# Performance work log

Hardware: AMD Instinct MI355X
Metric: run time of the kernel (lower is better)

Reference implementation:

```python
import jax, jax.numpy as jnp
import numpy as np

B, T, C, H, E, TOP_K = 4, 2048, 1024, 4096, 8, 2


def setup_inputs() -> dict:
    key = jax.random.key(0)
    k0, k1, k2, k3 = jax.random.split(key, 4)
    x = jax.random.normal(k0, (B, T, C), dtype=jnp.float32)
    Wr = jax.random.normal(k1, (C, E), dtype=jnp.float32) * (C ** -0.5)   # router
    W1 = jax.random.normal(k2, (E, C, H), dtype=jnp.float32) * (C ** -0.5)  # expert up-proj
    W2 = jax.random.normal(k3, (E, H, C), dtype=jnp.float32) * (H ** -0.5)  # expert down-proj
    return {"x": x, "Wr": Wr, "W1": W1, "W2": W2}


def reference(x, Wr, W1, W2):
    # x: (B, T, C) -> flatten to tokens, as the wrapper does (n_tokens = B*T)
    Bx, Tx, Cx = x.shape
    flat = x.reshape(-1, Cx)                      # (N, C)
    N = flat.shape[0]

    # --- routing (forward_topk): top-k gates, normalized (is_shared=False) ---
    logits = flat @ Wr                            # (N, E)
    top_vals, top_idx = jax.lax.top_k(logits, TOP_K)   # (N, k)
    gates = jax.nn.softmax(top_vals, axis=-1)     # normalizer = softmax over selected

    # dense combine matrix: gate weight per (token, expert), zero if not routed
    comb = jnp.zeros((N, E), dtype=flat.dtype)
    comb = comb.at[jnp.arange(N)[:, None], top_idx].set(gates)  # (N, E)

    # --- expert FFNs + weighted scatter-add combine ---
    def body(acc, params):
        W1e, W2e, we = params                     # (C,H), (H,C), (N,)
        h = jax.nn.gelu(flat @ W1e)               # (N, H)
        return acc + we[:, None] * (h @ W2e), None

    out, _ = jax.lax.scan(body, jnp.zeros_like(flat), (W1, W2, comb.T))
    return out.reshape(Bx, Tx, Cx)
```

## Files before the change

kernel.cpp:

```cpp
#include <hip/hip_runtime.h>

#define N_TOK 8192
#define CDIM  1024
#define HDIM  4096
#define NEXP  8
#define TOPK  2
#define ROWS  (N_TOK*TOPK)

#define BM 128
#define BN 128
#define BK 64
#define LDK 72

typedef short short8 __attribute__((ext_vector_type(8)));
typedef float floatx4 __attribute__((ext_vector_type(4)));

__device__ __forceinline__ unsigned short f2bf(float f){
  union { float f; unsigned int u; } v; v.f = f;
  unsigned int u = v.u;
  return (unsigned short)((u + 0x7fffu + ((u >> 16) & 1u)) >> 16);
}

__device__ __forceinline__ float gelu_tanh(float x){
  float u = 0.7978845608028654f * (x + 0.044715f * x * x * x);
  float s = __fdividef(1.f, 1.f + __expf(-2.f * u));
  return x * s;
}

__global__ void transpose_cast(const float* __restrict__ src,
                               unsigned short* __restrict__ dst,
                               int roff, int RP, int lds_, int coff, int CP,
                               size_t srcEsz){
  __shared__ __align__(16) unsigned short tile[64][72];
  const int e = blockIdx.z;
  const float* s = src + (size_t)e * srcEsz;
  unsigned short* d = dst + (size_t)e * (size_t)RP * (size_t)CP;
  const int c0 = blockIdx.x * 64, r0 = blockIdx.y * 64;
  const int tid = threadIdx.x;
  #pragma unroll
  for (int i = 0; i < 2; i++){
    int r  = (tid >> 3) + i * 32;
    int cc = (tid & 7) * 8;
    const float* p = s + (size_t)(roff + r0 + r) * lds_ + coff + c0 + cc;
    float4 v0 = *(const float4*)p;
    float4 v1 = *(const float4*)(p + 4);
    unsigned short t8[8];
    t8[0]=f2bf(v0.x); t8[1]=f2bf(v0.y); t8[2]=f2bf(v0.z); t8[3]=f2bf(v0.w);
    t8[4]=f2bf(v1.x); t8[5]=f2bf(v1.y); t8[6]=f2bf(v1.z); t8[7]=f2bf(v1.w);
    *(uint4*)&tile[r][cc] = *(uint4*)t8;
  }
  __syncthreads();
  #pragma unroll
  for (int i = 0; i < 2; i++){
    int oc = (tid >> 3) + i * 32;
    int rr = (tid & 7) * 8;
    unsigned short tmp[8];
    #pragma unroll
    for (int j = 0; j < 8; j++) tmp[j] = tile[rr + j][oc];
    *(uint4*)(d + (size_t)(c0 + oc) * RP + r0 + rr) = *(uint4*)tmp;
  }
}

__global__ void router_topk(const float* __restrict__ x,
                            const float* __restrict__ Wr,
                            int* __restrict__ cnt,
                            int* __restrict__ top_e,
                            float* __restrict__ top_g){
  const int lane = threadIdx.x & 63;
  const int wv   = threadIdx.x >> 6;
  const int t    = blockIdx.x * 4 + wv;
  const float* xr = x + (size_t)t * CDIM;
  float p[NEXP];
  #pragma unroll
  for (int e = 0; e < NEXP; e++) p[e] = 0.f;
  for (int c = lane; c < CDIM; c += 64){
    float xv = xr[c];
    float4 w0 = *(const float4*)(Wr + c * NEXP);
    float4 w1 = *(const float4*)(Wr + c * NEXP + 4);
    p[0] = fmaf(xv, w0.x, p[0]); p[1] = fmaf(xv, w0.y, p[1]);
    p[2] = fmaf(xv, w0.z, p[2]); p[3] = fmaf(xv, w0.w, p[3]);
    p[4] = fmaf(xv, w1.x, p[4]); p[5] = fmaf(xv, w1.y, p[5]);
    p[6] = fmaf(xv, w1.z, p[6]); p[7] = fmaf(xv, w1.w, p[7]);
  }
  #pragma unroll
  for (int e = 0; e < NEXP; e++){
    #pragma unroll
    for (int off = 32; off > 0; off >>= 1)
      p[e] += __shfl_xor(p[e], off, 64);
  }
  if (lane == 0){
    int e0 = 0; float v0 = p[0];
    #pragma unroll
    for (int e = 1; e < NEXP; e++) if (p[e] > v0){ v0 = p[e]; e0 = e; }
    int e1 = -1; float v1 = -1e30f;
    #pragma unroll
    for (int e = 0; e < NEXP; e++) if (e != e0 && p[e] > v1){ v1 = p[e]; e1 = e; }
    float ex  = __expf(v1 - v0);
    float inv = 1.f / (1.f + ex);
    top_e[t * 2 + 0] = e0; top_e[t * 2 + 1] = e1;
    top_g[t * 2 + 0] = inv; top_g[t * 2 + 1] = ex * inv;
    atomicAdd(&cnt[e0], 1);
    atomicAdd(&cnt[e1], 1);
  }
}

__global__ void scan_offsets(const int* __restrict__ cnt,
                             int* __restrict__ off,
                             int* __restrict__ cursor){
  if (threadIdx.x == 0){
    int s = 0;
    for (int e = 0; e < NEXP; e++){ off[e] = s; s += cnt[e]; cursor[e] = 0; }
  }
}

__global__ void assign_rows(const int* __restrict__ off, int* __restrict__ cursor,
                            const int* __restrict__ top_e, const float* __restrict__ top_g,
                            int* __restrict__ tok_of_row, float* __restrict__ gate_of_row){
  int t = blockIdx.x * blockDim.x + threadIdx.x;
  if (t >= N_TOK) return;
  #pragma unroll
  for (int k = 0; k < TOPK; k++){
    int e = top_e[t * 2 + k];
    int pos = atomicAdd(&cursor[e], 1);
    int r = off[e] + pos;
    tok_of_row[r]  = t;
    gate_of_row[r] = top_g[t * 2 + k];
  }
}

__global__ __launch_bounds__(256, 2)
void gemm1_expert(const float* __restrict__ x,
                  const unsigned short* __restrict__ w1t,
                  const int* __restrict__ cnt, const int* __restrict__ off,
                  const int* __restrict__ tok_of_row,
                  unsigned short* __restrict__ hbuf,
                  int HP){
  const int e  = blockIdx.z;
  const int m  = cnt[e];
  const int mt = blockIdx.y;
  if (mt * BM >= m) return;
  const int nt   = blockIdx.x;
  const int base = off[e];

  __shared__ __align__(16) unsigned short As[BM * LDK];
  __shared__ __align__(16) unsigned short Bs[BN * LDK];

  const int tid = threadIdx.x;
  const int lane = tid & 63, wv = tid >> 6;
  const int wm = wv & 1, wn = wv >> 1;
  const int q = lane >> 4, l16 = lane & 15;

  floatx4 acc[4][4];
  #pragma unroll
  for (int i = 0; i < 4; i++)
    #pragma unroll
    for (int j = 0; j < 4; j++) acc[i][j] = (floatx4){0.f, 0.f, 0.f, 0.f};

  const unsigned short* bsrc = w1t + ((size_t)e * HP + (size_t)nt * BN) * CDIM;

  int tokr[4];
  #pragma unroll
  for (int i = 0; i < 4; i++){
    int row  = (tid + i * 256) >> 3;
    int grow = mt * BM + row;
    tokr[i] = tok_of_row[base + (grow < m ? grow : 0)];
  }

  for (int kb = 0; kb < CDIM; kb += BK){
    #pragma unroll
    for (int i = 0; i < 4; i++){
      int chunk = tid + i * 256;
      int row = chunk >> 3;
      int kc  = (chunk & 7) * 8;
      const float* p = x + (size_t)tokr[i] * CDIM + kb + kc;
      float4 v0 = *(const float4*)p;
      float4 v1 = *(const float4*)(p + 4);
      unsigned short t8[8];
      t8[0]=f2bf(v0.x); t8[1]=f2bf(v0.y); t8[2]=f2bf(v0.z); t8[3]=f2bf(v0.w);
      t8[4]=f2bf(v1.x); t8[5]=f2bf(v1.y); t8[6]=f2bf(v1.z); t8[7]=f2bf(v1.w);
      *(uint4*)&As[row * LDK + kc] = *(uint4*)t8;
    }
    #pragma unroll
    for (int i = 0; i < 4; i++){
      int chunk = tid + i * 256;
      int row = chunk >> 3;
      int kc  = (chunk & 7) * 8;
      uint4 v = *(const uint4*)(bsrc + (size_t)row * CDIM + kb + kc);
      *(uint4*)&Bs[row * LDK + kc] = v;
    }
    __syncthreads();
    #pragma unroll
    for (int ks = 0; ks < BK; ks += 32){
      short8 a[4], b[4];
      #pragma unroll
      for (int i = 0; i < 4; i++)
        a[i] = *(const short8*)&As[(wm * 64 + i * 16 + l16) * LDK + ks + q * 8];
      #pragma unroll
      for (int j = 0; j < 4; j++)
        b[j] = *(const short8*)&Bs[(wn * 64 + j * 16 + l16) * LDK + ks + q * 8];
      #pragma unroll
      for (int i = 0; i < 4; i++)
        #pragma unroll
        for (int j = 0; j < 4; j++)
          acc[i][j] = __builtin_amdgcn_mfma_f32_16x16x32_bf16(a[i], b[j], acc[i][j], 0, 0, 0);
    }
    __syncthreads();
  }

  #pragma unroll
  for (int i = 0; i < 4; i++){
    #pragma unroll
    for (int r = 0; r < 4; r++){
      int row  = wm * 64 + i * 16 + q * 4 + r;
      int grow = mt * BM + row;
      if (grow < m){
        size_t hrow = (size_t)(base + grow) * HP + (size_t)nt * BN;
        #pragma unroll
        for (int j = 0; j < 4; j++){
          float g = gelu_tanh(acc[i][j][r]);
          hbuf[hrow + wn * 64 + j * 16 + l16] = f2bf(g);
        }
      }
    }
  }
}

__global__ __launch_bounds__(256, 2)
void gemm2_expert(const unsigned short* __restrict__ hbuf,
                  const unsigned short* __restrict__ w2t,
                  const int* __restrict__ cnt, const int* __restrict__ off,
                  const int* __restrict__ tok_of_row, const float* __restrict__ gate_of_row,
                  float* __restrict__ out,
                  int HP){
  const int e  = blockIdx.z;
  const int m  = cnt[e];
  const int mt = blockIdx.y;
  if (mt * BM >= m) return;
  const int nt   = blockIdx.x;
  const int base = off[e];

  __shared__ __align__(16) unsigned short As[BM * LDK];
  __shared__ __align__(16) unsigned short Bs[BN * LDK];

  const int tid = threadIdx.x;
  const int lane = tid & 63, wv = tid >> 6;
  const int wm = wv & 1, wn = wv >> 1;
  const int q = lane >> 4, l16 = lane & 15;

  floatx4 acc[4][4];
  #pragma unroll
  for (int i = 0; i < 4; i++)
    #pragma unroll
    for (int j = 0; j < 4; j++) acc[i][j] = (floatx4){0.f, 0.f, 0.f, 0.f};

  const unsigned short* bsrc = w2t + ((size_t)e * CDIM + (size_t)nt * BN) * HP;

  int arow[4];
  #pragma unroll
  for (int i = 0; i < 4; i++){
    int row  = (tid + i * 256) >> 3;
    int grow = mt * BM + row;
    arow[i] = base + (grow < m ? grow : 0);
  }

  for (int kb = 0; kb < HP; kb += BK){
    #pragma unroll
    for (int i = 0; i < 4; i++){
      int chunk = tid + i * 256;
      int row = chunk >> 3;
      int kc  = (chunk & 7) * 8;
      uint4 v = *(const uint4*)(hbuf + (size_t)arow[i] * HP + kb + kc);
      *(uint4*)&As[row * LDK + kc] = v;
    }
    #pragma unroll
    for (int i = 0; i < 4; i++){
      int chunk = tid + i * 256;
      int row = chunk >> 3;
      int kc  = (chunk & 7) * 8;
      uint4 v = *(const uint4*)(bsrc + (size_t)row * HP + kb + kc);
      *(uint4*)&Bs[row * LDK + kc] = v;
    }
    __syncthreads();
    #pragma unroll
    for (int ks = 0; ks < BK; ks += 32){
      short8 a[4], b[4];
      #pragma unroll
      for (int i = 0; i < 4; i++)
        a[i] = *(const short8*)&As[(wm * 64 + i * 16 + l16) * LDK + ks + q * 8];
      #pragma unroll
      for (int j = 0; j < 4; j++)
        b[j] = *(const short8*)&Bs[(wn * 64 + j * 16 + l16) * LDK + ks + q * 8];
      #pragma unroll
      for (int i = 0; i < 4; i++)
        #pragma unroll
        for (int j = 0; j < 4; j++)
          acc[i][j] = __builtin_amdgcn_mfma_f32_16x16x32_bf16(a[i], b[j], acc[i][j], 0, 0, 0);
    }
    __syncthreads();
  }

  #pragma unroll
  for (int i = 0; i < 4; i++){
    #pragma unroll
    for (int r = 0; r < 4; r++){
      int row  = wm * 64 + i * 16 + q * 4 + r;
      int grow = mt * BM + row;
      if (grow < m){
        int gr = base + grow;
        int tok = tok_of_row[gr];
        float gate = gate_of_row[gr];
        float* orow = out + (size_t)tok * CDIM + (size_t)nt * BN;
        #pragma unroll
        for (int j = 0; j < 4; j++)
          atomicAdd(&orow[wn * 64 + j * 16 + l16], acc[i][j][r] * gate);
      }
    }
  }
}

extern "C" void kernel_launch(void* const* d_in, const int* in_sizes, int n_in,
                              void* d_out, int out_size, void* d_ws, size_t ws_size,
                              hipStream_t stream) {
  const float* x  = (const float*)d_in[0];
  const float* Wr = (const float*)d_in[1];
  const float* W1 = (const float*)d_in[2];
  const float* W2 = (const float*)d_in[3];
  float* out = (float*)d_out;

  hipMemsetAsync(out, 0, (size_t)N_TOK * CDIM * sizeof(float), stream);

  const size_t META_SZ = 1u << 20;
  int P = -1;
  for (int cand = 1; cand <= 32; cand <<= 1){
    int HPc = HDIM / cand;
    size_t need = META_SZ
                + (size_t)ROWS * HPc * 2
                + (size_t)NEXP * HPc * CDIM * 2;
    if (need <= ws_size){ P = cand; break; }
  }
  if (P < 0){
    return;
  }
  const int HP = HDIM / P;

  char* ws = (char*)d_ws;
  int*   cnt         = (int*)ws;
  int*   off         = cnt + 8;
  int*   cursor      = off + 8;
  int*   tok_of_row  = (int*)(ws + 1024);
  float* gate_of_row = (float*)(ws + 1024 + 65536);
  int*   top_e       = (int*)(ws + 1024 + 131072);
  float* top_g       = (float*)(ws + 1024 + 196608);

  unsigned short* hbuf = (unsigned short*)(ws + META_SZ);
  unsigned short* wreg = (unsigned short*)(ws + META_SZ + (size_t)ROWS * HP * 2);

  hipMemsetAsync(cnt, 0, 96, stream);

  router_topk<<<dim3(N_TOK/4), 256, 0, stream>>>(x, Wr, cnt, top_e, top_g);
  scan_offsets<<<1, 64, 0, stream>>>(cnt, off, cursor);
  assign_rows<<<dim3(N_TOK/256), 256, 0, stream>>>(off, cursor, top_e, top_g,
                                                   tok_of_row, gate_of_row);

  for (int p = 0; p < P; p++){
    const int h0 = p * HP;
    transpose_cast<<<dim3(HP/64, CDIM/64, NEXP), 256, 0, stream>>>(
        W1, wreg, 0, CDIM, HDIM, h0, HP,
        (size_t)CDIM * HDIM);
    gemm1_expert<<<dim3(HP/BN, ROWS/BM, NEXP), 256, 0, stream>>>(
        x, wreg, cnt, off, tok_of_row, hbuf, HP);
    transpose_cast<<<dim3(CDIM/64, HP/64, NEXP), 256, 0, stream>>>(
        W2, wreg, h0, HP, CDIM, 0, CDIM,
        (size_t)HDIM * CDIM);
    gemm2_expert<<<dim3(CDIM/BN, ROWS/BM, NEXP), 256, 0, stream>>>(
        hbuf, wreg, cnt, off, tok_of_row, gate_of_row, out, HP);
  }
}
```

Measured before the change: 1.205 ms.

## Pre-cast x to bf16 and stage GEMM tiles via direct global-to-LDS loads with XOR swizzle

Adds a cast_x kernel that converts x to bf16 once, so gemm1 stops loading fp32 and converting the same token rows in every N-tile block. Both expert GEMMs now fill shared memory with global_load_lds 16-byte direct loads instead of going through registers. The padded LDS layout is replaced by an unpadded one with an XOR swizzle to avoid bank conflicts. This costs an extra workspace buffer and one more kernel launch, and relies on the swizzle matching the MFMA read pattern.

Result: faster. 1.008 ms (-16.3%).

```diff
diff --git a/kernel.cpp b/kernel.cpp
--- a/kernel.cpp
+++ b/kernel.cpp
@@ -10,10 +10,16 @@
 #define BM 128
 #define BN 128
 #define BK 64
-#define LDK 72
 
 typedef short short8 __attribute__((ext_vector_type(8)));
 typedef float floatx4 __attribute__((ext_vector_type(4)));
+
+typedef __attribute__((address_space(3))) unsigned int       as3_u32;
+typedef __attribute__((address_space(1))) const unsigned int as1_u32;
+
+__device__ __forceinline__ void gld16(const unsigned short* g, unsigned short* l){
+  __builtin_amdgcn_global_load_lds((as1_u32*)g, (as3_u32*)l, 16, 0, 0);
+}
 
 __device__ __forceinline__ unsigned short f2bf(float f){
   union { float f; unsigned int u; } v; v.f = f;
@@ -25,6 +31,14 @@
   float u = 0.7978845608028654f * (x + 0.044715f * x * x * x);
   float s = __fdividef(1.f, 1.f + __expf(-2.f * u));
   return x * s;
+}
+
+__global__ void cast_x(const float4* __restrict__ in, uint2* __restrict__ out){
+  int i = blockIdx.x * 256 + threadIdx.x;
+  float4 v = in[i];
+  unsigned short t[4];
+  t[0] = f2bf(v.x); t[1] = f2bf(v.y); t[2] = f2bf(v.z); t[3] = f2bf(v.w);
+  out[i] = *(uint2*)t;
 }
 
 __global__ void transpose_cast(const float* __restrict__ src,
@@ -129,7 +143,7 @@
 }
 
 __global__ __launch_bounds__(256, 2)
-void gemm1_expert(const float* __restrict__ x,
+void gemm1_expert(const unsigned short* __restrict__ xbf,
                   const unsigned short* __restrict__ w1t,
                   const int* __restrict__ cnt, const int* __restrict__ off,
                   const int* __restrict__ tok_of_row,
@@ -142,13 +156,33 @@
   const int nt   = blockIdx.x;
   const int base = off[e];
 
-  __shared__ __align__(16) unsigned short As[BM * LDK];
-  __shared__ __align__(16) unsigned short Bs[BN * LDK];
+  __shared__ __align__(16) unsigned short As[BM * BK];
+  __shared__ __align__(16) unsigned short Bs[BN * BK];
 
   const int tid = threadIdx.x;
-  const int lane = tid & 63, wv = tid >> 6;
-  const int wm = wv & 1, wn = wv >> 1;
+  const int lane = tid & 63, w = tid >> 6;
+  const int wm = w & 1, wn = w >> 1;
   const int q = lane >> 4, l16 = lane & 15;
+  const int sw = l16 & 7;
+
+  const unsigned short* bsrc = w1t + ((size_t)e * HP + (size_t)nt * BN) * CDIM;
+
+  const unsigned short* agp[4];
+  const unsigned short* bgp[4];
+  unsigned short* lA[4];
+  unsigned short* lB[4];
+  #pragma unroll
+  for (int it = 0; it < 4; it++){
+    int r = w * 32 + it * 8 + (lane >> 3);
+    int g = (lane & 7) ^ (r & 7);
+    int grow = mt * BM + r;
+    int cr   = grow < m ? grow : (m - 1);
+    int tok  = tok_of_row[base + cr];
+    agp[it] = xbf + (size_t)tok * CDIM + g * 8;
+    bgp[it] = bsrc + (size_t)r * CDIM + g * 8;
+    lA[it]  = &As[(w * 32 + it * 8) * BK];
+    lB[it]  = &Bs[(w * 32 + it * 8) * BK];
+  }
 
   floatx4 acc[4][4];
   #pragma unroll
@@ -156,48 +190,22 @@
     #pragma unroll
     for (int j = 0; j < 4; j++) acc[i][j] = (floatx4){0.f, 0.f, 0.f, 0.f};
 
-  const unsigned short* bsrc = w1t + ((size_t)e * HP + (size_t)nt * BN) * CDIM;
-
-  int tokr[4];
-  #pragma unroll
-  for (int i = 0; i < 4; i++){
-    int row  = (tid + i * 256) >> 3;
-    int grow = mt * BM + row;
-    tokr[i] = tok_of_row[base + (grow < m ? grow : 0)];
-  }
-
   for (int kb = 0; kb < CDIM; kb += BK){
     #pragma unroll
-    for (int i = 0; i < 4; i++){
-      int chunk = tid + i * 256;
-      int row = chunk >> 3;
-      int kc  = (chunk & 7) * 8;
-      const float* p = x + (size_t)tokr[i] * CDIM + kb + kc;
-      float4 v0 = *(const float4*)p;
-      float4 v1 = *(const float4*)(p + 4);
-      unsigned short t8[8];
-      t8[0]=f2bf(v0.x); t8[1]=f2bf(v0.y); t8[2]=f2bf(v0.z); t8[3]=f2bf(v0.w);
-      t8[4]=f2bf(v1.x); t8[5]=f2bf(v1.y); t8[6]=f2bf(v1.z); t8[7]=f2bf(v1.w);
-      *(uint4*)&As[row * LDK + kc] = *(uint4*)t8;
-    }
-    #pragma unroll
-    for (int i = 0; i < 4; i++){
-      int chunk = tid + i * 256;
-      int row = chunk >> 3;
-      int kc  = (chunk & 7) * 8;
-      uint4 v = *(const uint4*)(bsrc + (size_t)row * CDIM + kb + kc);
-      *(uint4*)&Bs[row * LDK + kc] = v;
-    }
+    for (int it = 0; it < 4; it++) gld16(agp[it] + kb, lA[it]);
+    #pragma unroll
+    for (int it = 0; it < 4; it++) gld16(bgp[it] + kb, lB[it]);
     __syncthreads();
     #pragma unroll
     for (int ks = 0; ks < BK; ks += 32){
+      const int cb = ks >> 3;
       short8 a[4], b[4];
       #pragma unroll
       for (int i = 0; i < 4; i++)
-        a[i] = *(const short8*)&As[(wm * 64 + i * 16 + l16) * LDK + ks + q * 8];
+        a[i] = *(const short8*)&As[(wm * 64 + i * 16 + l16) * BK + (((q + cb) ^ sw) * 8)];
       #pragma unroll
       for (int j = 0; j < 4; j++)
-        b[j] = *(const short8*)&Bs[(wn * 64 + j * 16 + l16) * LDK + ks + q * 8];
+        b[j] = *(const short8*)&Bs[(wn * 64 + j * 16 + l16) * BK + (((q + cb) ^ sw) * 8)];
       #pragma unroll
       for (int i = 0; i < 4; i++)
         #pragma unroll
@@ -217,8 +225,8 @@
         size_t hrow = (size_t)(base + grow) * HP + (size_t)nt * BN;
         #pragma unroll
         for (int j = 0; j < 4; j++){
-          float g = gelu_tanh(acc[i][j][r]);
-          hbuf[hrow + wn * 64 + j * 16 + l16] = f2bf(g);
+          float gv = gelu_tanh(acc[i][j][r]);
+          hbuf[hrow + wn * 64 + j * 16 + l16] = f2bf(gv);
         }
       }
     }
@@ -239,13 +247,32 @@
   const int nt   = blockIdx.x;
   const int base = off[e];
 
-  __shared__ __align__(16) unsigned short As[BM * LDK];
-  __shared__ __align__(16) unsigned short Bs[BN * LDK];
+  __shared__ __align__(16) unsigned short As[BM * BK];
+  __shared__ __align__(16) unsigned short Bs[BN * BK];
 
   const int tid = threadIdx.x;
-  const int lane = tid & 63, wv = tid >> 6;
-  const int wm = wv & 1, wn = wv >> 1;
+  const int lane = tid & 63, w = tid >> 6;
+  const int wm = w & 1, wn = w >> 1;
   const int q = lane >> 4, l16 = lane & 15;
+  const int sw = l16 & 7;
+
+  const unsigned short* bsrc = w2t + ((size_t)e * CDIM + (size_t)nt * BN) * HP;
+
+  const unsigned short* agp[4];
+  const unsigned short* bgp[4];
+  unsigned short* lA[4];
+  unsigned short* lB[4];
+  #pragma unroll
+  for (int it = 0; it < 4; it++){
+    int r = w * 32 + it * 8 + (lane >> 3);
+    int g = (lane & 7) ^ (r & 7);
+    int grow = mt * BM + r;
+    int cr   = grow < m ? grow : (m - 1);
+    agp[it] = hbuf + (size_t)(base + cr) * HP + g * 8;
+    bgp[it] = bsrc + (size_t)r * HP + g * 8;
+    lA[it]  = &As[(w * 32 + it * 8) * BK];
+    lB[it]  = &Bs[(w * 32 + it * 8) * BK];
+  }
 
   floatx4 acc[4][4];
   #pragma unroll
@@ -253,43 +280,22 @@
     #pragma unroll
     for (int j = 0; j < 4; j++) acc[i][j] = (floatx4){0.f, 0.f, 0.f, 0.f};
 
-  const unsigned short* bsrc = w2t + ((size_t)e * CDIM + (size_t)nt * BN) * HP;
-
-  int arow[4];
-  #pragma unroll
-  for (int i = 0; i < 4; i++){
-    int row  = (tid + i * 256) >> 3;
-    int grow = mt * BM + row;
-    arow[i] = base + (grow < m ? grow : 0);
-  }
-
   for (int kb = 0; kb < HP; kb += BK){
     #pragma unroll
-    for (int i = 0; i < 4; i++){
-      int chunk = tid + i * 256;
-      int row = chunk >> 3;
-      int kc  = (chunk & 7) * 8;
-      uint4 v = *(const uint4*)(hbuf + (size_t)arow[i] * HP + kb + kc);
-      *(uint4*)&As[row * LDK + kc] = v;
-    }
-    #pragma unroll
-    for (int i = 0; i < 4; i++){
-      int chunk = tid + i * 256;
-      int row = chunk >> 3;
-      int kc  = (chunk & 7) * 8;
-      uint4 v = *(const uint4*)(bsrc + (size_t)row * HP + kb + kc);
-      *(uint4*)&Bs[row * LDK + kc] = v;
-    }
+    for (int it = 0; it < 4; it++) gld16(agp[it] + kb, lA[it]);
+    #pragma unroll
+    for (int it = 0; it < 4; it++) gld16(bgp[it] + kb, lB[it]);
     __syncthreads();
     #pragma unroll
     for (int ks = 0; ks < BK; ks += 32){
+      const int cb = ks >> 3;
       short8 a[4], b[4];
       #pragma unroll
       for (int i = 0; i < 4; i++)
-        a[i] = *(const short8*)&As[(wm * 64 + i * 16 + l16) * LDK + ks + q * 8];
+        a[i] = *(const short8*)&As[(wm * 64 + i * 16 + l16) * BK + (((q + cb) ^ sw) * 8)];
       #pragma unroll
       for (int j = 0; j < 4; j++)
-        b[j] = *(const short8*)&Bs[(wn * 64 + j * 16 + l16) * LDK + ks + q * 8];
+        b[j] = *(const short8*)&Bs[(wn * 64 + j * 16 + l16) * BK + (((q + cb) ^ sw) * 8)];
       #pragma unroll
       for (int i = 0; i < 4; i++)
         #pragma unroll
@@ -330,17 +336,16 @@
   hipMemsetAsync(out, 0, (size_t)N_TOK * CDIM * sizeof(float), stream);
 
   const size_t META_SZ = 1u << 20;
+  const size_t XBF_SZ  = (size_t)N_TOK * CDIM * 2;
   int P = -1;
   for (int cand = 1; cand <= 32; cand <<= 1){
     int HPc = HDIM / cand;
-    size_t need = META_SZ
+    size_t need = META_SZ + XBF_SZ
                 + (size_t)ROWS * HPc * 2
                 + (size_t)NEXP * HPc * CDIM * 2;
     if (need <= ws_size){ P = cand; break; }
   }
-  if (P < 0){
-    return;
-  }
+  if (P < 0) return;
   const int HP = HDIM / P;
 
   char* ws = (char*)d_ws;
@@ -352,11 +357,13 @@
   int*   top_e       = (int*)(ws + 1024 + 131072);
   float* top_g       = (float*)(ws + 1024 + 196608);
 
-  unsigned short* hbuf = (unsigned short*)(ws + META_SZ);
-  unsigned short* wreg = (unsigned short*)(ws + META_SZ + (size_t)ROWS * HP * 2);
+  unsigned short* xbf  = (unsigned short*)(ws + META_SZ);
+  unsigned short* hbuf = (unsigned short*)(ws + META_SZ + XBF_SZ);
+  unsigned short* wreg = (unsigned short*)(ws + META_SZ + XBF_SZ + (size_t)ROWS * HP * 2);
 
   hipMemsetAsync(cnt, 0, 96, stream);
 
+  cast_x<<<dim3(N_TOK*CDIM/4/256), 256, 0, stream>>>((const float4*)x, (uint2*)xbf);
   router_topk<<<dim3(N_TOK/4), 256, 0, stream>>>(x, Wr, cnt, top_e, top_g);
   scan_offsets<<<1, 64, 0, stream>>>(cnt, off, cursor);
   assign_rows<<<dim3(N_TOK/256), 256, 0, stream>>>(off, cursor, top_e, top_g,
@@ -368,7 +375,7 @@
         W1, wreg, 0, CDIM, HDIM, h0, HP,
         (size_t)CDIM * HDIM);
     gemm1_expert<<<dim3(HP/BN, ROWS/BM, NEXP), 256, 0, stream>>>(
-        x, wreg, cnt, off, tok_of_row, hbuf, HP);
+        xbf, wreg, cnt, off, tok_of_row, hbuf, HP);
     transpose_cast<<<dim3(CDIM/64, HP/64, NEXP), 256, 0, stream>>>(
         W2, wreg, h0, HP, CDIM, 0, CDIM,
         (size_t)HDIM * CDIM);
```
